# Kernel tuning notes

Hardware: AMD Instinct MI355X
Metric: run time of the kernel (lower is better)

Reference implementation:

```python
import jax, jax.numpy as jnp
import numpy as np

B, T, D = 64, 2048, 512


def setup_inputs() -> dict:
    key = jax.random.key(0)
    ks = jax.random.split(key, 6)
    lim_tau = 1.0 / np.sqrt(2 * D)  # torch Linear default init bound
    lim_mem = 1.0 / np.sqrt(D)
    return {
        "x": jax.random.normal(ks[0], (B, T, D), dtype=jnp.float32),
        "tau_w": jax.random.uniform(ks[1], (D, 2 * D), jnp.float32, -lim_tau, lim_tau),
        "tau_b": jax.random.uniform(ks[2], (D,), jnp.float32, -lim_tau, lim_tau),
        "mem_w": jax.random.uniform(ks[3], (D, D), jnp.float32, -lim_mem, lim_mem),
        "mem_b": jax.random.uniform(ks[4], (D,), jnp.float32, -lim_mem, lim_mem),
        "log_thresh": jnp.zeros((D,), jnp.float32),
    }


def reference(x, tau_w, tau_b, mem_w, mem_b, log_thresh):
    b, t, d = x.shape
    thr = jax.nn.sigmoid(log_thresh)  # [D]

    def step(carry, xt):
        v, tau = carry  # each [B, D]
        # liquid time-constant gate: sigmoid(Linear([xt, tau]))
        tau = jax.nn.sigmoid(jnp.concatenate([xt, tau], axis=-1) @ tau_w.T + tau_b)
        alpha = jnp.exp(-1.0 / (tau + 1e-6))
        v = alpha * v + (1.0 - alpha) * (xt @ mem_w.T + mem_b)
        s = (v >= thr).astype(x.dtype)  # spike
        v = v * (1.0 - s)  # hard reset
        return (v, tau), s

    x_tbd = jnp.swapaxes(x, 0, 1)  # [T, B, D] for scan
    init = (jnp.zeros((b, d), x.dtype), jnp.ones((b, d), x.dtype))
    (v, tau), spikes = jax.lax.scan(step, init, x_tbd)
    return jnp.swapaxes(spikes, 0, 1), tau, v  # [B,T,D], [B,D], [B,D]
```

## Files before the change

### kernel.cpp

```cpp
#include <hip/hip_runtime.h>
#include <math.h>

#define B_ 64
#define T_ 2048
#define D_ 512
#define BT_ (B_ * T_)
#define XWORDS (B_ * D_)

typedef unsigned long long u64;

__global__ void prep_weights(const float* __restrict__ tau_w,
                             const float* __restrict__ mem_w,
                             float* __restrict__ Wcat,
                             float* __restrict__ WTh) {
    int idx = blockIdx.x * 256 + threadIdx.x;
    {
        int k = idx >> 10, j = idx & 1023;
        float v = (j < 512) ? tau_w[j * 1024 + k] : mem_w[(j - 512) * 512 + k];
        Wcat[idx] = v;
    }
    if (idx < 512 * 512) {
        int k = idx >> 9, d = idx & 511;
        WTh[idx] = tau_w[d * 1024 + 512 + k];
    }
}

__global__ __launch_bounds__(256, 2)
void gemm_xw(const float* __restrict__ X, const float* __restrict__ Wc,
             const float* __restrict__ tau_b, const float* __restrict__ mem_b,
             float* __restrict__ Aout, float* __restrict__ Mout) {
    __shared__ __align__(16) float As[16][128];
    __shared__ __align__(16) float Bs[16][128];
    const int bn = blockIdx.x;
    const int bm = blockIdx.y;
    const int tid = threadIdx.x;
    const int tm = (tid >> 4) << 3;
    const int tn = (tid & 15) << 3;
    const int m0 = bm * 128, n0 = bn * 128;

    const float4* X4 = (const float4*)X;
    const float4* Wc4 = (const float4*)Wc;

    float acc[8][8];
#pragma unroll
    for (int i = 0; i < 8; i++)
#pragma unroll
        for (int j = 0; j < 8; j++) acc[i][j] = 0.0f;

    const int ar = tid >> 1;
    const int ac2 = (tid & 1) * 2;
    const int bkr = tid >> 4;
    const int bc = (tid & 15) * 2;

    for (int kt = 0; kt < 512; kt += 16) {
        float4 av0 = X4[(m0 + ar) * 128 + (kt >> 2) + ac2];
        float4 av1 = X4[(m0 + ar) * 128 + (kt >> 2) + ac2 + 1];
        float4 bv0 = Wc4[(kt + bkr) * 256 + bn * 32 + bc];
        float4 bv1 = Wc4[(kt + bkr) * 256 + bn * 32 + bc + 1];
        __syncthreads();
        As[ac2 * 4 + 0][ar] = av0.x;
        As[ac2 * 4 + 1][ar] = av0.y;
        As[ac2 * 4 + 2][ar] = av0.z;
        As[ac2 * 4 + 3][ar] = av0.w;
        As[ac2 * 4 + 4][ar] = av1.x;
        As[ac2 * 4 + 5][ar] = av1.y;
        As[ac2 * 4 + 6][ar] = av1.z;
        As[ac2 * 4 + 7][ar] = av1.w;
        *(float4*)&Bs[bkr][bc * 4] = bv0;
        *(float4*)&Bs[bkr][bc * 4 + 4] = bv1;
        __syncthreads();
#pragma unroll
        for (int kk = 0; kk < 16; kk++) {
            float4 a0 = *(const float4*)&As[kk][tm];
            float4 a1 = *(const float4*)&As[kk][tm + 4];
            float4 b0 = *(const float4*)&Bs[kk][tn];
            float4 b1 = *(const float4*)&Bs[kk][tn + 4];
            float av[8] = {a0.x, a0.y, a0.z, a0.w, a1.x, a1.y, a1.z, a1.w};
            float bv[8] = {b0.x, b0.y, b0.z, b0.w, b1.x, b1.y, b1.z, b1.w};
#pragma unroll
            for (int i = 0; i < 8; i++)
#pragma unroll
                for (int j = 0; j < 8; j++)
                    acc[i][j] = fmaf(av[i], bv[j], acc[i][j]);
        }
    }

    const bool isA = (bn < 4);
    float* Cout = isA ? Aout : Mout;
    const float* bias = isA ? tau_b : mem_b;
    const int ncol0 = (isA ? n0 : n0 - 512) + tn;
    float bj[8];
#pragma unroll
    for (int j = 0; j < 8; j++) bj[j] = bias[ncol0 + j];
#pragma unroll
    for (int i = 0; i < 8; i++) {
        size_t off = (size_t)(m0 + tm + i) * 512 + ncol0;
        float4 o0, o1;
        o0.x = acc[i][0] + bj[0]; o0.y = acc[i][1] + bj[1];
        o0.z = acc[i][2] + bj[2]; o0.w = acc[i][3] + bj[3];
        o1.x = acc[i][4] + bj[4]; o1.y = acc[i][5] + bj[5];
        o1.z = acc[i][6] + bj[6]; o1.w = acc[i][7] + bj[7];
        *(float4*)&Cout[off] = o0;
        *(float4*)&Cout[off + 4] = o1;
    }
}

__global__ void init_sync(u64* __restrict__ xchg, int* __restrict__ ctr) {
    int idx = blockIdx.x * 256 + threadIdx.x;
    if (idx < 2 * XWORDS) xchg[idx] = (idx < XWORDS) ? 0x3F800000ull : 0ull;
    if (idx < 16) ctr[idx] = 0;
}

__global__ __launch_bounds__(512)
__attribute__((amdgpu_waves_per_eu(2, 2)))
void scan_wave(const float* __restrict__ WTh,
               const float* __restrict__ Mm,
               const float* __restrict__ log_thresh,
               float* __restrict__ AmOut,
               float* __restrict__ OutTail,
               u64* __restrict__ xchg,
               int* __restrict__ ctr) {
    __shared__ __align__(16) float4 w_lds[8192];
    __shared__ __align__(16) float tau_s[2][512];
    __shared__ __align__(16) float part[2][16][64];
    __shared__ int role_s;

    const int tid = threadIdx.x;

    if (tid == 0) {
        unsigned xcd;
        asm volatile("s_getreg_b32 %0, hwreg(HW_REG_XCC_ID)" : "=s"(xcd));
        xcd &= 7;
        int rank = atomicAdd(&ctr[xcd], 1) & 31;
        role_s = ((rank & 7) << 8) | ((int)xcd * 4 + (rank >> 3));
    }
    __syncthreads();
    const int sg = role_s >> 8;
    const int bp = role_s & 255;

    {
        const int ch = tid & 63;
        const int kr8 = tid >> 6;
        float* wl = (float*)w_lds;
        for (int i = 0; i < 64; i++) {
            int krow = i * 8 + kr8;
            float val = WTh[krow * 512 + sg * 64 + ch];
            wl[(krow >> 2) * 256 + ch * 4 + (krow & 3)] = val;
        }
    }

    const int ws = tid >> 6;
    const int lane = tid & 63;
    const int cp = lane & 31;
    const int kh = lane >> 5;
    const bool self = (ws == sg);

    const int eb = tid >> 6;
    const int ech = tid & 63;
    const int gch = sg * 64 + ech;
    float thr = 0.f, v = 0.f, tau_keep = 0.f;
    if (tid < 128) thr = 1.0f / (1.0f + expf(-log_thresh[gch]));
    size_t abase = ((size_t)(bp * 2 + eb) * T_) * D_ + gch;

    if (tid < 128) tau_s[eb][sg * 64 + ech] = 1.0f;
    __syncthreads();

    for (int c = 1; c <= T_; c++) {
        float a_in = 0.f, m_in = 0.f;
        if (tid < 128) { a_in = AmOut[abase]; m_in = Mm[abase]; }

        if (!self) {
            const u64* s0 = xchg + (size_t)((c - 1) & 1) * XWORDS
                                 + (size_t)(bp * 2) * 512 + ws * 64 + lane;
            const u64* s1 = s0 + 512;
            const unsigned tgt = (unsigned)(c - 1);
            u64 v0, v1;
            int guard = 0;
            do {
                v0 = __hip_atomic_load(s0, __ATOMIC_RELAXED,
                                       __HIP_MEMORY_SCOPE_AGENT);
                v1 = __hip_atomic_load(s1, __ATOMIC_RELAXED,
                                       __HIP_MEMORY_SCOPE_AGENT);
            } while ((((unsigned)(v0 >> 32) < tgt) |
                      ((unsigned)(v1 >> 32) < tgt)) && ++guard < (1 << 22));
            tau_s[0][ws * 64 + lane] = __uint_as_float((unsigned)v0);
            tau_s[1][ws * 64 + lane] = __uint_as_float((unsigned)v1);
        }
        __builtin_amdgcn_wave_barrier();

        float acc00 = 0.f, acc01 = 0.f, acc10 = 0.f, acc11 = 0.f;
#pragma unroll
        for (int q = 0; q < 8; q++) {
            const int qq = ws * 16 + kh * 8 + q;
            float4 wA = w_lds[qq * 64 + cp];
            float4 wB = w_lds[qq * 64 + cp + 32];
            float4 t0 = *(const float4*)&tau_s[0][ws * 64 + kh * 32 + q * 4];
            float4 t1 = *(const float4*)&tau_s[1][ws * 64 + kh * 32 + q * 4];
            acc00 = fmaf(t0.x, wA.x, acc00); acc00 = fmaf(t0.y, wA.y, acc00);
            acc00 = fmaf(t0.z, wA.z, acc00); acc00 = fmaf(t0.w, wA.w, acc00);
            acc01 = fmaf(t0.x, wB.x, acc01); acc01 = fmaf(t0.y, wB.y, acc01);
            acc01 = fmaf(t0.z, wB.z, acc01); acc01 = fmaf(t0.w, wB.w, acc01);
            acc10 = fmaf(t1.x, wA.x, acc10); acc10 = fmaf(t1.y, wA.y, acc10);
            acc10 = fmaf(t1.z, wA.z, acc10); acc10 = fmaf(t1.w, wA.w, acc10);
            acc11 = fmaf(t1.x, wB.x, acc11); acc11 = fmaf(t1.y, wB.y, acc11);
            acc11 = fmaf(t1.z, wB.z, acc11); acc11 = fmaf(t1.w, wB.w, acc11);
        }
        const int slot = ws * 2 + kh;
        part[0][slot][cp]      = acc00;
        part[0][slot][cp + 32] = acc01;
        part[1][slot][cp]      = acc10;
        part[1][slot][cp + 32] = acc11;
        __syncthreads();

        if (tid < 128) {
            float sum = 0.f;
#pragma unroll
            for (int j = 0; j < 16; j++) sum += part[eb][j][ech];
            float pre = sum + a_in;
            float tau = 1.0f / (1.0f + expf(-pre));
            float alpha = expf(-1.0f / (tau + 1e-6f));
            v = alpha * v + (1.0f - alpha) * m_in;
            float s = (v >= thr) ? 1.0f : 0.0f;
            AmOut[abase] = s;
            v = v * (1.0f - s);
            tau_keep = tau;
            tau_s[eb][sg * 64 + ech] = tau;
            u64 pack = ((u64)(unsigned)c << 32) | (u64)__float_as_uint(tau);
            __hip_atomic_store(&xchg[(size_t)(c & 1) * XWORDS
                                     + (bp * 2 + eb) * 512 + gch],
                               pack, __ATOMIC_RELAXED, __HIP_MEMORY_SCOPE_AGENT);
            abase += D_;
        }
        __syncthreads();
    }

    if (tid < 128) {
        const size_t batch = bp * 2 + eb;
        OutTail[(size_t)BT_ * D_ + batch * D_ + gch] = tau_keep;
        OutTail[(size_t)BT_ * D_ + (size_t)B_ * D_ + batch * D_ + gch] = v;
    }
}

extern "C" void kernel_launch(void* const* d_in, const int* in_sizes, int n_in,
                              void* d_out, int out_size, void* d_ws, size_t ws_size,
                              hipStream_t stream) {
    (void)in_sizes; (void)n_in; (void)out_size; (void)ws_size;
    const float* x          = (const float*)d_in[0];
    const float* tau_w      = (const float*)d_in[1];
    const float* tau_b      = (const float*)d_in[2];
    const float* mem_w      = (const float*)d_in[3];
    const float* mem_b      = (const float*)d_in[4];
    const float* log_thresh = (const float*)d_in[5];
    float* out = (float*)d_out;

    float* Wcat = (float*)d_ws;
    float* WTh  = Wcat + 512 * 1024;
    float* Mout = WTh + 512 * 512;
    u64* xchg = (u64*)d_ws;
    int* ctr  = (int*)((char*)d_ws + 2 * XWORDS * sizeof(u64));

    float* Aout = out;

    prep_weights<<<2048, 256, 0, stream>>>(tau_w, mem_w, Wcat, WTh);
    gemm_xw<<<dim3(8, 1024), 256, 0, stream>>>(x, Wcat, tau_b, mem_b, Aout, Mout);
    init_sync<<<256, 256, 0, stream>>>(xchg, ctr);

    const float* WThc = WTh;
    const float* Mmc  = Mout;
    const float* ltc  = log_thresh;
    float* outp = out;
    u64* xchgp = xchg;
    int* ctrp = ctr;
    void* args[7] = {(void*)&WThc, (void*)&Mmc, (void*)&ltc,
                     (void*)&Aout, (void*)&outp, (void*)&xchgp, (void*)&ctrp};
    hipLaunchCooperativeKernel((const void*)scan_wave, dim3(256), dim3(512),
                               args, 0, stream);
}
```

Baseline: 5.411 ms.

## Hold recurrent weights in registers and broadcast tau via readlane

The per-step recurrent matvec now keeps each thread's 64-element weight column in VGPRs instead of LDS. Each wave's tau slice is broadcast across lanes with readlane rather than read from shared memory, so the partial-sum array shrinks to 8 slots. The next step's gate and membrane inputs are also prefetched one step ahead to hide global-load latency. A dummy padded LDS array is kept, presumably to hold occupancy at one block per CU, and the change raises register pressure (64 extra VGPRs plus 128 readlanes per step).

```diff
diff --git a/kernel.cpp b/kernel.cpp
--- a/kernel.cpp
+++ b/kernel.cpp
@@ -113,19 +113,20 @@
 
 __global__ __launch_bounds__(512)
 __attribute__((amdgpu_waves_per_eu(2, 2)))
-void scan_wave(const float* __restrict__ WTh,
-               const float* __restrict__ Mm,
-               const float* __restrict__ log_thresh,
-               float* __restrict__ AmOut,
-               float* __restrict__ OutTail,
-               u64* __restrict__ xchg,
-               int* __restrict__ ctr) {
-    __shared__ __align__(16) float4 w_lds[8192];
-    __shared__ __align__(16) float tau_s[2][512];
-    __shared__ __align__(16) float part[2][16][64];
+void scan_reg(const float* __restrict__ WTh,
+              const float* __restrict__ Mm,
+              const float* __restrict__ log_thresh,
+              float* __restrict__ AmOut,
+              float* __restrict__ OutTail,
+              u64* __restrict__ xchg,
+              int* __restrict__ ctr) {
+    __shared__ __align__(16) float part[2][8][64];
+    __shared__ __align__(16) float tau_sm[2][64];
     __shared__ int role_s;
+    __shared__ float4 pad_lds[7168];
 
     const int tid = threadIdx.x;
+    if (tid == 9999) ((volatile float*)pad_lds)[0] = 1.f;
 
     if (tid == 0) {
         unsigned xcd;
@@ -138,22 +139,20 @@
     const int sg = role_s >> 8;
     const int bp = role_s & 255;
 
-    {
-        const int ch = tid & 63;
-        const int kr8 = tid >> 6;
-        float* wl = (float*)w_lds;
-        for (int i = 0; i < 64; i++) {
-            int krow = i * 8 + kr8;
-            float val = WTh[krow * 512 + sg * 64 + ch];
-            wl[(krow >> 2) * 256 + ch * 4 + (krow & 3)] = val;
-        }
-    }
-
     const int ws = tid >> 6;
     const int lane = tid & 63;
-    const int cp = lane & 31;
-    const int kh = lane >> 5;
     const bool self = (ws == sg);
+
+    const float* wcol = WTh + sg * 64 + lane;
+    float4 w[16];
+#pragma unroll
+    for (int q4 = 0; q4 < 16; q4++) {
+        const int k0 = ws * 64 + q4 * 4;
+        w[q4].x = wcol[(size_t)(k0 + 0) * 512];
+        w[q4].y = wcol[(size_t)(k0 + 1) * 512];
+        w[q4].z = wcol[(size_t)(k0 + 2) * 512];
+        w[q4].w = wcol[(size_t)(k0 + 3) * 512];
+    }
 
     const int eb = tid >> 6;
     const int ech = tid & 63;
@@ -162,13 +161,20 @@
     if (tid < 128) thr = 1.0f / (1.0f + expf(-log_thresh[gch]));
     size_t abase = ((size_t)(bp * 2 + eb) * T_) * D_ + gch;
 
-    if (tid < 128) tau_s[eb][sg * 64 + ech] = 1.0f;
+    if (tid < 128) tau_sm[eb][ech] = 1.0f;
+
+    float a_pf = 0.f, m_pf = 0.f;
+    if (tid < 128) { a_pf = AmOut[abase]; m_pf = Mm[abase]; }
     __syncthreads();
 
     for (int c = 1; c <= T_; c++) {
-        float a_in = 0.f, m_in = 0.f;
-        if (tid < 128) { a_in = AmOut[abase]; m_in = Mm[abase]; }
-
+        float a_nx = 0.f, m_nx = 0.f;
+        if (tid < 128) {
+            size_t nx = (c < T_) ? abase + D_ : abase;
+            a_nx = AmOut[nx]; m_nx = Mm[nx];
+        }
+
+        float t0f, t1f;
         if (!self) {
             const u64* s0 = xchg + (size_t)((c - 1) & 1) * XWORDS
                                  + (size_t)(bp * 2) * 512 + ws * 64 + lane;
@@ -183,53 +189,54 @@
                                        __HIP_MEMORY_SCOPE_AGENT);
             } while ((((unsigned)(v0 >> 32) < tgt) |
                       ((unsigned)(v1 >> 32) < tgt)) && ++guard < (1 << 22));
-            tau_s[0][ws * 64 + lane] = __uint_as_float((unsigned)v0);
-            tau_s[1][ws * 64 + lane] = __uint_as_float((unsigned)v1);
-        }
-        __builtin_amdgcn_wave_barrier();
-
-        float acc00 = 0.f, acc01 = 0.f, acc10 = 0.f, acc11 = 0.f;
-#pragma unroll
-        for (int q = 0; q < 8; q++) {
-            const int qq = ws * 16 + kh * 8 + q;
-            float4 wA = w_lds[qq * 64 + cp];
-            float4 wB = w_lds[qq * 64 + cp + 32];
-            float4 t0 = *(const float4*)&tau_s[0][ws * 64 + kh * 32 + q * 4];
-            float4 t1 = *(const float4*)&tau_s[1][ws * 64 + kh * 32 + q * 4];
-            acc00 = fmaf(t0.x, wA.x, acc00); acc00 = fmaf(t0.y, wA.y, acc00);
-            acc00 = fmaf(t0.z, wA.z, acc00); acc00 = fmaf(t0.w, wA.w, acc00);
-            acc01 = fmaf(t0.x, wB.x, acc01); acc01 = fmaf(t0.y, wB.y, acc01);
-            acc01 = fmaf(t0.z, wB.z, acc01); acc01 = fmaf(t0.w, wB.w, acc01);
-            acc10 = fmaf(t1.x, wA.x, acc10); acc10 = fmaf(t1.y, wA.y, acc10);
-            acc10 = fmaf(t1.z, wA.z, acc10); acc10 = fmaf(t1.w, wA.w, acc10);
-            acc11 = fmaf(t1.x, wB.x, acc11); acc11 = fmaf(t1.y, wB.y, acc11);
-            acc11 = fmaf(t1.z, wB.z, acc11); acc11 = fmaf(t1.w, wB.w, acc11);
-        }
-        const int slot = ws * 2 + kh;
-        part[0][slot][cp]      = acc00;
-        part[0][slot][cp + 32] = acc01;
-        part[1][slot][cp]      = acc10;
-        part[1][slot][cp + 32] = acc11;
+            t0f = __uint_as_float((unsigned)v0);
+            t1f = __uint_as_float((unsigned)v1);
+        } else {
+            t0f = tau_sm[0][lane];
+            t1f = tau_sm[1][lane];
+        }
+        const int t0i = __float_as_int(t0f);
+        const int t1i = __float_as_int(t1f);
+
+        float acc0 = 0.f, acc1 = 0.f;
+#pragma unroll
+        for (int q4 = 0; q4 < 16; q4++) {
+#pragma unroll
+            for (int j = 0; j < 4; j++) {
+                const int kk = q4 * 4 + j;
+                const float wv = (j == 0) ? w[q4].x : (j == 1) ? w[q4].y
+                               : (j == 2) ? w[q4].z : w[q4].w;
+                float ta = __uint_as_float(
+                    (unsigned)__builtin_amdgcn_readlane(t0i, kk));
+                float tb = __uint_as_float(
+                    (unsigned)__builtin_amdgcn_readlane(t1i, kk));
+                acc0 = fmaf(ta, wv, acc0);
+                acc1 = fmaf(tb, wv, acc1);
+            }
+        }
+        part[0][ws][lane] = acc0;
+        part[1][ws][lane] = acc1;
         __syncthreads();
 
         if (tid < 128) {
             float sum = 0.f;
 #pragma unroll
-            for (int j = 0; j < 16; j++) sum += part[eb][j][ech];
-            float pre = sum + a_in;
+            for (int j = 0; j < 8; j++) sum += part[eb][j][ech];
+            float pre = sum + a_pf;
             float tau = 1.0f / (1.0f + expf(-pre));
             float alpha = expf(-1.0f / (tau + 1e-6f));
-            v = alpha * v + (1.0f - alpha) * m_in;
+            v = alpha * v + (1.0f - alpha) * m_pf;
             float s = (v >= thr) ? 1.0f : 0.0f;
             AmOut[abase] = s;
             v = v * (1.0f - s);
             tau_keep = tau;
-            tau_s[eb][sg * 64 + ech] = tau;
+            tau_sm[eb][ech] = tau;
             u64 pack = ((u64)(unsigned)c << 32) | (u64)__float_as_uint(tau);
             __hip_atomic_store(&xchg[(size_t)(c & 1) * XWORDS
                                      + (bp * 2 + eb) * 512 + gch],
                                pack, __ATOMIC_RELAXED, __HIP_MEMORY_SCOPE_AGENT);
             abase += D_;
+            a_pf = a_nx; m_pf = m_nx;
         }
         __syncthreads();
     }
@@ -273,6 +280,6 @@
     int* ctrp = ctr;
     void* args[7] = {(void*)&WThc, (void*)&Mmc, (void*)&ltc,
                      (void*)&Aout, (void*)&outp, (void*)&xchgp, (void*)&ctrp};
-    hipLaunchCooperativeKernel((const void*)scan_wave, dim3(256), dim3(512),
+    hipLaunchCooperativeKernel((const void*)scan_reg, dim3(256), dim3(512),
                                args, 0, stream);
 }
```

New measurement: 5.861 ms. 8.3% more time.
